# Kernel tuning notes

Hardware: AMD Instinct MI355X
Metric: run time of the kernel (lower is better)

The kernel has to match this reference:

```python
import jax, jax.numpy as jnp
import numpy as np

B, T, DM = 1, 8192, 1024
DS, DC, EXP = 16, 4, 2
DI = DM * EXP  # 2048


def setup_inputs() -> dict:
    key = jax.random.key(0)
    ks = jax.random.split(key, 6)
    sc = lambda k, shape, s: jax.random.normal(k, shape, jnp.float32) * s
    return {
        "x": jax.random.normal(ks[0], (B, T, DM), jnp.float32),
        "W_in": sc(ks[1], (DM, 2 * DI), 0.02),        # stored [in, out]
        "conv_w": sc(ks[2], (DI, 1, DC), 0.2),        # depthwise conv weight (OIH)
        "conv_b": jnp.zeros((DI,), jnp.float32),
        "W_x": sc(ks[3], (DI, 2 * DS + 1), 0.02),     # stored [in, out]
        "A_log": jnp.log(jnp.arange(1, DS + 1, dtype=jnp.float32)),
        "D": jnp.ones((DI,), jnp.float32),
        "W_out": sc(ks[4], (DI, DM), 0.02),           # stored [in, out]
    }


def reference(x, W_in, conv_w, conv_b, W_x, A_log, D, W_out):
    Bq, Tq, _ = x.shape
    # input projection and gate split
    xz = x @ W_in                              # [B,T,2*DI]
    xc, z = jnp.split(xz, 2, axis=-1)          # each [B,T,DI]
    # causal depthwise conv1d (pad left DC-1 == torch pad both + truncate [:T])
    xcT = jnp.transpose(xc, (0, 2, 1))         # [B,DI,T]
    conv = jax.lax.conv_general_dilated(
        xcT, conv_w, window_strides=(1,), padding=[(DC - 1, 0)],
        feature_group_count=DI)
    conv = conv + conv_b[None, :, None]
    xs = jax.nn.silu(jnp.transpose(conv, (0, 2, 1)))   # [B,T,DI]
    # selective SSM parameters (single shared delta per timestep)
    x_dbl = xs @ W_x                           # [B,T,2N+1]
    delta = jax.nn.softplus(x_dbl[..., :1])    # [B,T,1]
    Bp = x_dbl[..., 1:1 + DS]                  # [B,T,N]
    Cp = x_dbl[..., 1 + DS:]                   # [B,T,N]
    A = -jnp.exp(A_log)                        # [N]
    A_bar = jnp.exp(delta * A)                 # [B,T,N]
    B_bar = delta * Bp                         # [B,T,N]

    def step(h, inp):
        a_t, b_t, x_t, c_t = inp               # [B,N],[B,N],[B,DI],[B,N]
        h = a_t[:, None, :] * h + b_t[:, None, :] * x_t[:, :, None]  # [B,DI,N]
        y_t = jnp.einsum('bdn,bn->bd', h, c_t)
        return h, y_t

    h0 = jnp.zeros((Bq, DI, DS), xs.dtype)
    seq = (jnp.swapaxes(A_bar, 0, 1), jnp.swapaxes(B_bar, 0, 1),
           jnp.swapaxes(xs, 0, 1), jnp.swapaxes(Cp, 0, 1))
    _, ys = jax.lax.scan(step, h0, seq)        # ys: [T,B,DI]
    y = jnp.swapaxes(ys, 0, 1) + D * xs        # [B,T,DI]
    y = y * jax.nn.silu(z)
    return y @ W_out                           # [B,T,DM]
```

## Files before the change

### kernel.cpp

```cpp
#include <hip/hip_runtime.h>
#include <hip/hip_bf16.h>

#define T_SEQ 8192
#define DMODEL 1024
#define DINNER 2048
#define NSTATE 16
#define NCH 128
#define CL 64

typedef __attribute__((ext_vector_type(8))) short bf16x8;
typedef __attribute__((ext_vector_type(4))) float f32x4;

__device__ __forceinline__ float bf2f(ushort u) {
  union { unsigned u; float f; } c; c.u = ((unsigned)u) << 16; return c.f;
}
__device__ __forceinline__ ushort f2bf(float f) {
  union { float f; unsigned u; } c; c.f = f;
  unsigned r = c.u + 0x7FFFu + ((c.u >> 16) & 1u);
  return (ushort)(r >> 16);
}

#define GLD16(dst, src) __builtin_amdgcn_global_load_lds( \
    (const __attribute__((address_space(1))) void*)(src), \
    (__attribute__((address_space(3))) void*)(dst), 16, 0, 0)

template<int N> __device__ __forceinline__ void waitcnt_vm() {
  asm volatile("s_waitcnt vmcnt(%0)" :: "i"(N) : "memory");
}
#define LGKM0() do { asm volatile("s_waitcnt lgkmcnt(0)" ::: "memory"); \
                     __builtin_amdgcn_sched_barrier(0); } while (0)
#define BAR() do { __builtin_amdgcn_sched_barrier(0); __builtin_amdgcn_s_barrier(); \
                   __builtin_amdgcn_sched_barrier(0); } while (0)

__global__ __launch_bounds__(256) void cast_bf16(const float* __restrict__ in,
                                                 ushort* __restrict__ out, int n4) {
  int i = blockIdx.x * 256 + threadIdx.x;
  if (i < n4) {
    float4 v = ((const float4*)in)[i];
    ushort4 o;
    o.x = f2bf(v.x); o.y = f2bf(v.y); o.z = f2bf(v.z); o.w = f2bf(v.w);
    ((ushort4*)out)[i] = o;
  }
}

__global__ __launch_bounds__(256) void transpose_bf16(const float* __restrict__ in,
                                                      ushort* __restrict__ out, int R, int C) {
  __shared__ float tile[32][33];
  int bx = blockIdx.x * 32;
  int by = blockIdx.y * 32;
  int x = threadIdx.x, y = threadIdx.y;
#pragma unroll
  for (int j = 0; j < 32; j += 8)
    tile[y + j][x] = in[(size_t)(by + y + j) * C + bx + x];
  __syncthreads();
#pragma unroll
  for (int j = 0; j < 32; j += 8)
    out[(size_t)(bx + y + j) * R + by + x] = f2bf(tile[x][y + j]);
}

__global__ __launch_bounds__(256) void wx_transpose_pad(const float* __restrict__ Wx,
                                                        ushort* __restrict__ wxT) {
  int idx = blockIdx.x * 256 + threadIdx.x;
  int j = idx >> 11;
  int k = idx & 2047;
  wxT[idx] = (j < 33) ? f2bf(Wx[k * 33 + j]) : (ushort)0;
}

template<int OUTMODE, int MR>
__global__ __launch_bounds__(512, 2)
void gemm8p(const ushort* __restrict__ A, const ushort* __restrict__ B,
            void* __restrict__ out0, void* __restrict__ out1,
            int N, int K, int MX) {
  constexpr int BM = MR * 32;
  constexpr int H = MR / 2;
  constexpr int AHL = BM / 128;
  constexpr int VM = 2 * AHL + 2;
  extern __shared__ __align__(16) char smem[];
  char* const sBr = smem + 2 * BM * 128;

  const int tid = threadIdx.x, lane = tid & 63, wid = tid >> 6;
  const int wm = wid >> 2, wn = wid & 3;
  const int xcd = blockIdx.x & 7, jb = blockIdx.x >> 3;
  const int mtile = xcd * MX + (jb % MX), ntile = jb / MX;
  const int mbase = mtile * BM, nbase = ntile * 256;
  const int NT = K >> 6;

  const int sr = tid >> 3;
  const int scol = ((tid & 7) ^ (sr & 7)) << 3;
  const ushort* pA = A + (size_t)(mbase + sr) * K + scol;
  const ushort* pB = B + (size_t)(nbase + sr) * K + scol;

  auto stgA = [&](int buf, int h, int tt) {
#pragma unroll
    for (int r = 0; r < AHL; ++r)
      GLD16(smem + buf * (BM * 128) + (h * (BM / 2) + r * 64) * 128 + wid * 1024,
            pA + (size_t)(h * (BM / 2) + r * 64) * K + (size_t)tt * 64);
  };
  auto stgB = [&](int buf, int h, int tt) {
#pragma unroll
    for (int r = 0; r < 2; ++r)
      GLD16(sBr + buf * 32768 + (h * 128 + r * 64) * 128 + wid * 1024,
            pB + (size_t)(h * 128 + r * 64) * K + (size_t)tt * 64);
  };

  const int frow = lane & 15, hh = lane >> 4;
  const int sw[2] = { ((hh) ^ (frow & 7)) << 4, ((4 + hh) ^ (frow & 7)) << 4 };
  const int arow = (wm * (MR * 16) + frow) * 128;
  const int brow = (wn * 64 + frow) * 128;

  f32x4 acc[MR][4];
#pragma unroll
  for (int m = 0; m < MR; ++m)
#pragma unroll
    for (int n = 0; n < 4; ++n) acc[m][n] = (f32x4){0.f, 0.f, 0.f, 0.f};

  stgA(0, 0, 0); stgA(0, 1, 0); stgB(0, 0, 0); stgB(0, 1, 0);
  if (NT > 1) { stgA(1, 0, 1); stgA(1, 1, 1); stgB(1, 0, 1); }
  waitcnt_vm<VM>();
  BAR();

  for (int t = 0; t < NT; ++t) {
    const int b = t & 1;
    const char* bA = smem + b * (BM * 128);
    const char* bB = sBr + b * 32768;
    bf16x8 alo[H][2], ahi[H][2], b01[2][2], b23[2][2];

#pragma unroll
    for (int m = 0; m < H; ++m)
#pragma unroll
      for (int kk = 0; kk < 2; ++kk)
        alo[m][kk] = *(const bf16x8*)(bA + arow + m * 2048 + sw[kk]);
#pragma unroll
    for (int n = 0; n < 2; ++n)
#pragma unroll
      for (int kk = 0; kk < 2; ++kk)
        b01[n][kk] = *(const bf16x8*)(bB + brow + n * 2048 + sw[kk]);
    if (t + 1 < NT) stgB((t + 1) & 1, 1, t + 1);
    BAR(); LGKM0();
    __builtin_amdgcn_s_setprio(1);
#pragma unroll
    for (int m = 0; m < H; ++m)
#pragma unroll
      for (int n = 0; n < 2; ++n)
#pragma unroll
        for (int kk = 0; kk < 2; ++kk)
          acc[m][n] = __builtin_amdgcn_mfma_f32_16x16x32_bf16(alo[m][kk], b01[n][kk], acc[m][n], 0, 0, 0);
    __builtin_amdgcn_s_setprio(0);
    BAR();

#pragma unroll
    for (int m = 0; m < H; ++m)
#pragma unroll
      for (int kk = 0; kk < 2; ++kk)
        ahi[m][kk] = *(const bf16x8*)(bA + arow + (H + m) * 2048 + sw[kk]);
    BAR(); LGKM0();
    __builtin_amdgcn_s_setprio(1);
#pragma unroll
    for (int m = 0; m < H; ++m)
#pragma unroll
      for (int n = 0; n < 2; ++n)
#pragma unroll
        for (int kk = 0; kk < 2; ++kk)
          acc[H + m][n] = __builtin_amdgcn_mfma_f32_16x16x32_bf16(ahi[m][kk], b01[n][kk], acc[H + m][n], 0, 0, 0);
    __builtin_amdgcn_s_setprio(0);
    BAR();

#pragma unroll
    for (int n = 0; n < 2; ++n)
#pragma unroll
      for (int kk = 0; kk < 2; ++kk)
        b23[n][kk] = *(const bf16x8*)(bB + brow + (2 + n) * 2048 + sw[kk]);
    if (t + 2 < NT) stgA(b, 0, t + 2);
    BAR(); LGKM0();
    __builtin_amdgcn_s_setprio(1);
#pragma unroll
    for (int m = 0; m < H; ++m)
#pragma unroll
      for (int n = 0; n < 2; ++n)
#pragma unroll
        for (int kk = 0; kk < 2; ++kk)
          acc[H + m][2 + n] = __builtin_amdgcn_mfma_f32_16x16x32_bf16(ahi[m][kk], b23[n][kk], acc[H + m][2 + n], 0, 0, 0);
    __builtin_amdgcn_s_setprio(0);
    BAR();

    if (t + 2 < NT) { stgA(b, 1, t + 2); stgB(b, 0, t + 2); }
    __builtin_amdgcn_s_setprio(1);
#pragma unroll
    for (int m = 0; m < H; ++m)
#pragma unroll
      for (int n = 0; n < 2; ++n)
#pragma unroll
        for (int kk = 0; kk < 2; ++kk)
          acc[m][2 + n] = __builtin_amdgcn_mfma_f32_16x16x32_bf16(alo[m][kk], b23[n][kk], acc[m][2 + n], 0, 0, 0);
    __builtin_amdgcn_s_setprio(0);
    if (t + 2 < NT) waitcnt_vm<VM>(); else waitcnt_vm<0>();
    BAR();
  }

  const int crow0 = mbase + wm * (MR * 16) + (lane >> 4) * 4;
  const int ccol0 = wn * 64 + (lane & 15);
  if (OUTMODE == 0) {
    float* po = (float*)out0;
#pragma unroll
    for (int m = 0; m < MR; ++m)
#pragma unroll
      for (int n = 0; n < 4; ++n)
#pragma unroll
        for (int j = 0; j < 4; ++j)
          po[(size_t)(crow0 + m * 16 + j) * N + nbase + ccol0 + n * 16] = acc[m][n][j];
  } else {
    ushort* dst = (nbase < 2048) ? (ushort*)out0 : (ushort*)out1;
    const int cbase = (nbase & 2047) + ccol0;
#pragma unroll
    for (int m = 0; m < MR; ++m)
#pragma unroll
      for (int n = 0; n < 4; ++n)
#pragma unroll
        for (int j = 0; j < 4; ++j)
          dst[(size_t)(crow0 + m * 16 + j) * 2048 + cbase + n * 16] = f2bf(acc[m][n][j]);
  }
}

__global__ __launch_bounds__(256) void gemm_thin(const ushort* __restrict__ A,
                                                 const ushort* __restrict__ Bw,
                                                 float* __restrict__ part) {
  __shared__ __align__(16) ushort sA[128 * 64];
  __shared__ __align__(16) ushort sB[48 * 64];
  const int tid = threadIdx.x, lane = tid & 63, wid = tid >> 6;
  const int mbase = blockIdx.x * 128;
  const int kbase = blockIdx.y * 512;
  const int frow = lane & 15, fke = (lane >> 4) * 8;

  f32x4 acc[2][3];
#pragma unroll
  for (int m = 0; m < 2; ++m)
#pragma unroll
    for (int n = 0; n < 3; ++n) acc[m][n] = (f32x4){0.f, 0.f, 0.f, 0.f};

  for (int k0 = 0; k0 < 512; k0 += 64) {
#pragma unroll
    for (int j = 0; j < 4; ++j) {
      int o = tid * 16 + j * 4096;
      int row = o >> 7, ke = ((o >> 4) & 7) * 8;
      GLD16((char*)sA + wid * 1024 + j * 4096,
            A + (size_t)(mbase + row) * DINNER + kbase + k0 + ke);
    }
    for (int i = tid; i < 384; i += 256) {
      int brow = i >> 3, kc = (i & 7) * 8;
      *(bf16x8*)&sB[brow * 64 + kc] = *(const bf16x8*)(Bw + (size_t)brow * DINNER + kbase + k0 + kc);
    }
    __syncthreads();
    bf16x8 af[2][2], bf_[3][2];
#pragma unroll
    for (int m = 0; m < 2; ++m)
#pragma unroll
      for (int ks = 0; ks < 2; ++ks)
        af[m][ks] = *(const bf16x8*)&sA[(wid * 32 + m * 16 + frow) * 64 + ks * 32 + fke];
#pragma unroll
    for (int n = 0; n < 3; ++n)
#pragma unroll
      for (int ks = 0; ks < 2; ++ks)
        bf_[n][ks] = *(const bf16x8*)&sB[(n * 16 + frow) * 64 + ks * 32 + fke];
#pragma unroll
    for (int m = 0; m < 2; ++m)
#pragma unroll
      for (int n = 0; n < 3; ++n)
#pragma unroll
        for (int ks = 0; ks < 2; ++ks)
          acc[m][n] = __builtin_amdgcn_mfma_f32_16x16x32_bf16(af[m][ks], bf_[n][ks], acc[m][n], 0, 0, 0);
    __syncthreads();
  }
  float* po = part + (size_t)blockIdx.y * (T_SEQ * 48);
#pragma unroll
  for (int m = 0; m < 2; ++m)
#pragma unroll
    for (int n = 0; n < 3; ++n)
#pragma unroll
      for (int j = 0; j < 4; ++j) {
        int rr = mbase + wid * 32 + m * 16 + (lane >> 4) * 4 + j;
        int cc = n * 16 + (lane & 15);
        po[(size_t)rr * 48 + cc] = acc[m][n][j];
      }
}

__global__ __launch_bounds__(256) void reduce4(const float* __restrict__ part,
                                               float* __restrict__ xdbl) {
  int i = blockIdx.x * 256 + threadIdx.x;
  const float4* p = (const float4*)part;
  float4 a = p[i], b = p[i + 98304], c = p[i + 2 * 98304], d = p[i + 3 * 98304];
  ((float4*)xdbl)[i] = make_float4(a.x + b.x + c.x + d.x, a.y + b.y + c.y + d.y,
                                   a.z + b.z + c.z + d.z, a.w + b.w + c.w + d.w);
}

__global__ __launch_bounds__(256) void conv_silu(const ushort* __restrict__ xc,
                                                 const float* __restrict__ cw,
                                                 const float* __restrict__ cb,
                                                 ushort* __restrict__ xs) {
  int idx = blockIdx.x * 256 + threadIdx.x;
  int t = idx >> 11, d = idx & 2047;
  float4 w = *(const float4*)(cw + d * 4);
  float a = cb[d];
  const float wk[4] = {w.x, w.y, w.z, w.w};
#pragma unroll
  for (int k = 0; k < 4; ++k) {
    int tt = t - 3 + k;
    if (tt >= 0) a += bf2f(xc[(size_t)tt * 2048 + d]) * wk[k];
  }
  float s = a / (1.f + expf(-a));
  xs[idx] = f2bf(s);
}

__global__ __launch_bounds__(256) void precompute_k(const float* __restrict__ xdbl,
                                                    const float* __restrict__ A_log,
                                                    float* __restrict__ abar,
                                                    float* __restrict__ bbar,
                                                    float* __restrict__ cc,
                                                    float* __restrict__ dlt) {
  int t = blockIdx.x * 256 + threadIdx.x;
  if (t >= T_SEQ) return;
  const float* r = xdbl + (size_t)t * 48;
  float v = r[0];
  float delta = (v > 20.f) ? v : log1pf(expf(v));
  dlt[t] = delta;
#pragma unroll
  for (int n = 0; n < NSTATE; ++n) {
    float A = -expf(A_log[n]);
    abar[t * 16 + n] = expf(delta * A);
    bbar[t * 16 + n] = delta * r[1 + n];
    cc[t * 16 + n]   = r[17 + n];
  }
}

__global__ __launch_bounds__(256) void chunkprod_k(const float* __restrict__ dlt,
                                                   const float* __restrict__ A_log,
                                                   float* __restrict__ P) {
  int idx = blockIdx.x * 256 + threadIdx.x;
  if (idx >= NCH * NSTATE) return;
  int c = idx >> 4, n = idx & 15;
  float s = 0.f;
  for (int i = 0; i < CL; ++i) s += dlt[c * CL + i];
  P[idx] = expf(-expf(A_log[n]) * s);
}

__global__ __launch_bounds__(256) void scan1(const ushort* __restrict__ xs,
                                             const float* __restrict__ abar,
                                             const float* __restrict__ bbar,
                                             float* __restrict__ hend) {
  int c = blockIdx.x;
  int d = blockIdx.y * 256 + threadIdx.x;
  __shared__ float s_ab[CL * 16], s_bb[CL * 16];
  for (int e = threadIdx.x; e < CL * 16; e += 256) {
    s_ab[e] = abar[(size_t)c * CL * 16 + e];
    s_bb[e] = bbar[(size_t)c * CL * 16 + e];
  }
  __syncthreads();
  float h[16];
#pragma unroll
  for (int n = 0; n < 16; ++n) h[n] = 0.f;
  int tbase = c * CL;
  for (int i = 0; i < CL; ++i) {
    float x = bf2f(xs[(size_t)(tbase + i) * DINNER + d]);
#pragma unroll
    for (int n = 0; n < 16; ++n) h[n] = s_ab[i * 16 + n] * h[n] + s_bb[i * 16 + n] * x;
  }
  float* o = hend + ((size_t)c * DINNER + d) * 16;
#pragma unroll
  for (int qq = 0; qq < 4; ++qq)
    ((float4*)o)[qq] = make_float4(h[4 * qq], h[4 * qq + 1], h[4 * qq + 2], h[4 * qq + 3]);
}

__global__ __launch_bounds__(256) void scan2(const float* __restrict__ hend,
                                             const float* __restrict__ P,
                                             float* __restrict__ hin) {
  int idx = blockIdx.x * 256 + threadIdx.x;
  int n = idx & 15;
  float h = 0.f;
  for (int c = 0; c < NCH; ++c) {
    hin[(size_t)c * (DINNER * 16) + idx] = h;
    h = P[c * 16 + n] * h + hend[(size_t)c * (DINNER * 16) + idx];
  }
}

__global__ __launch_bounds__(256) void scan3(const ushort* __restrict__ xs,
                                             const ushort* __restrict__ zb,
                                             const float* __restrict__ abar,
                                             const float* __restrict__ bbar,
                                             const float* __restrict__ cc,
                                             const float* __restrict__ hin,
                                             const float* __restrict__ Dv,
                                             ushort* __restrict__ y) {
  int c = blockIdx.x;
  int d = blockIdx.y * 256 + threadIdx.x;
  __shared__ float s_ab[CL * 16], s_bb[CL * 16], s_cc[CL * 16];
  for (int e = threadIdx.x; e < CL * 16; e += 256) {
    s_ab[e] = abar[(size_t)c * CL * 16 + e];
    s_bb[e] = bbar[(size_t)c * CL * 16 + e];
    s_cc[e] = cc[(size_t)c * CL * 16 + e];
  }
  __syncthreads();
  float h[16];
  const float* hi = hin + ((size_t)c * DINNER + d) * 16;
#pragma unroll
  for (int qq = 0; qq < 4; ++qq) {
    float4 v = ((const float4*)hi)[qq];
    h[4 * qq] = v.x; h[4 * qq + 1] = v.y; h[4 * qq + 2] = v.z; h[4 * qq + 3] = v.w;
  }
  float Dd = Dv[d];
  int tbase = c * CL;
  for (int i = 0; i < CL; ++i) {
    size_t t = tbase + i;
    float x = bf2f(xs[t * DINNER + d]);
    float ys = 0.f;
#pragma unroll
    for (int n = 0; n < 16; ++n) {
      h[n] = s_ab[i * 16 + n] * h[n] + s_bb[i * 16 + n] * x;
      ys += s_cc[i * 16 + n] * h[n];
    }
    float z = bf2f(zb[t * 2048 + d]);
    float yv = (ys + Dd * x) * (z / (1.f + expf(-z)));
    y[t * DINNER + d] = f2bf(yv);
  }
}

extern "C" void kernel_launch(void* const* d_in, const int* in_sizes, int n_in,
                              void* d_out, int out_size, void* d_ws, size_t ws_size,
                              hipStream_t stream) {
  const float* x      = (const float*)d_in[0];
  const float* W_in   = (const float*)d_in[1];
  const float* conv_w = (const float*)d_in[2];
  const float* conv_b = (const float*)d_in[3];
  const float* W_x    = (const float*)d_in[4];
  const float* A_log  = (const float*)d_in[5];
  const float* Dv     = (const float*)d_in[6];
  const float* W_out  = (const float*)d_in[7];
  float* out = (float*)d_out;

  char* w = (char*)d_ws;
  auto alloc = [&](size_t bytes) { char* p = w; w += (bytes + 255) & ~(size_t)255; return p; };

  ushort* xbf   = (ushort*)alloc((size_t)T_SEQ * DMODEL * 2);
  ushort* winT  = (ushort*)alloc((size_t)4096 * 1024 * 2);
  ushort* woutT = (ushort*)alloc((size_t)1024 * 2048 * 2);
  ushort* wxT   = (ushort*)alloc((size_t)48 * 2048 * 2);
  ushort* xc    = (ushort*)alloc((size_t)T_SEQ * DINNER * 2);
  ushort* zb    = (ushort*)alloc((size_t)T_SEQ * DINNER * 2);
  ushort* xs    = (ushort*)alloc((size_t)T_SEQ * DINNER * 2);
  float*  xdbl  = (float*) alloc((size_t)T_SEQ * 48 * 4);
  float*  parts = (float*) alloc((size_t)4 * T_SEQ * 48 * 4);
  float*  abar  = (float*) alloc((size_t)T_SEQ * 16 * 4);
  float*  bbar  = (float*) alloc((size_t)T_SEQ * 16 * 4);
  float*  ccb   = (float*) alloc((size_t)T_SEQ * 16 * 4);
  float*  dlt   = (float*) alloc((size_t)T_SEQ * 4);
  float*  P     = (float*) alloc((size_t)NCH * 16 * 4);
  float*  hend  = (float*) alloc((size_t)NCH * DINNER * 16 * 4);
  float*  hin   = (float*) alloc((size_t)NCH * DINNER * 16 * 4);
  ushort* ybf   = (ushort*)alloc((size_t)T_SEQ * DINNER * 2);

  auto kg1 = gemm8p<1, 8>;
  auto kg3 = gemm8p<0, 4>;
  hipFuncSetAttribute(reinterpret_cast<const void*>(kg1),
                      hipFuncAttributeMaxDynamicSharedMemorySize, 131072);
  hipFuncSetAttribute(reinterpret_cast<const void*>(kg3),
                      hipFuncAttributeMaxDynamicSharedMemorySize, 98304);

  cast_bf16<<<(T_SEQ * DMODEL / 4 + 255) / 256, 256, 0, stream>>>(x, xbf, T_SEQ * DMODEL / 4);
  transpose_bf16<<<dim3(4096 / 32, 1024 / 32), dim3(32, 8), 0, stream>>>(W_in, winT, 1024, 4096);
  transpose_bf16<<<dim3(1024 / 32, 2048 / 32), dim3(32, 8), 0, stream>>>(W_out, woutT, 2048, 1024);
  wx_transpose_pad<<<(48 * 2048) / 256, 256, 0, stream>>>(W_x, wxT);

  kg1<<<dim3(512), 512, 131072, stream>>>(xbf, winT, xc, zb, 4096, 1024, 4);

  conv_silu<<<(T_SEQ * DINNER) / 256, 256, 0, stream>>>(xc, conv_w, conv_b, xs);

  gemm_thin<<<dim3(T_SEQ / 128, 4), 256, 0, stream>>>(xs, wxT, parts);
  reduce4<<<(T_SEQ * 48 / 4) / 256, 256, 0, stream>>>(parts, xdbl);

  precompute_k<<<T_SEQ / 256, 256, 0, stream>>>(xdbl, A_log, abar, bbar, ccb, dlt);
  chunkprod_k<<<(NCH * 16 + 255) / 256, 256, 0, stream>>>(dlt, A_log, P);

  scan1<<<dim3(NCH, DINNER / 256), 256, 0, stream>>>(xs, abar, bbar, hend);
  scan2<<<(DINNER * 16) / 256, 256, 0, stream>>>(hend, P, hin);
  scan3<<<dim3(NCH, DINNER / 256), 256, 0, stream>>>(xs, zb, abar, bbar, ccb, hin, Dv, ybf);

  kg3<<<dim3(256), 512, 98304, stream>>>(ybf, woutT, out, nullptr, 1024, 2048, 8);
}
```

Before: 298.6 us.

## Fuse prep kernels, fold reduce/chunkprod into precompute, store chunk states as bf16

Merges the cast and the three weight-transpose kernels into one launch, and folds the partial-sum reduction and the chunk decay-product computation into precompute_k using a shared-memory stage and wave shuffles. The inter-chunk states hend/hin are stored in bf16 instead of fp32. scan2 now batches its loads across 8 chunks at a time to give more memory-level parallelism. The aim is fewer launches and less memory traffic, in exchange for lower precision of the carried SSM state and a precompute launch of only 32 blocks.

```diff
diff --git a/kernel.cpp b/kernel.cpp
--- a/kernel.cpp
+++ b/kernel.cpp
@@ -29,41 +29,46 @@
 }
 #define LGKM0() do { asm volatile("s_waitcnt lgkmcnt(0)" ::: "memory"); \
                      __builtin_amdgcn_sched_barrier(0); } while (0)
-#define BAR() do { __builtin_amdgcn_sched_barrier(0); __builtin_amdgcn_s_barrier(); \
+#define BAR() do { __builtin_amdgcn_s_barrier(); \
                    __builtin_amdgcn_sched_barrier(0); } while (0)
 
-__global__ __launch_bounds__(256) void cast_bf16(const float* __restrict__ in,
-                                                 ushort* __restrict__ out, int n4) {
-  int i = blockIdx.x * 256 + threadIdx.x;
-  if (i < n4) {
-    float4 v = ((const float4*)in)[i];
+__global__ __launch_bounds__(256) void prep_all(const float* __restrict__ x,
+                                                const float* __restrict__ W_in,
+                                                const float* __restrict__ W_out,
+                                                const float* __restrict__ Wx,
+                                                ushort* __restrict__ xbf,
+                                                ushort* __restrict__ winT,
+                                                ushort* __restrict__ woutT,
+                                                ushort* __restrict__ wxT) {
+  __shared__ float tile[32][33];
+  int b = blockIdx.x, tid = threadIdx.x;
+  if (b < 8192) {
+    int i = b * 256 + tid;
+    float4 v = ((const float4*)x)[i];
     ushort4 o;
     o.x = f2bf(v.x); o.y = f2bf(v.y); o.z = f2bf(v.z); o.w = f2bf(v.w);
-    ((ushort4*)out)[i] = o;
-  }
-}
-
-__global__ __launch_bounds__(256) void transpose_bf16(const float* __restrict__ in,
-                                                      ushort* __restrict__ out, int R, int C) {
-  __shared__ float tile[32][33];
-  int bx = blockIdx.x * 32;
-  int by = blockIdx.y * 32;
-  int x = threadIdx.x, y = threadIdx.y;
+    ((ushort4*)xbf)[i] = o;
+    return;
+  }
+  b -= 8192;
+  const float* in; ushort* out; int R, C, bx, by;
+  if (b < 4096)      { in = W_in;  out = winT;  R = 1024; C = 4096; bx = b & 127; by = b >> 7; }
+  else if (b < 6144) { b -= 4096; in = W_out; out = woutT; R = 2048; C = 1024; bx = b & 31; by = b >> 5; }
+  else {
+    int idx = (b - 6144) * 256 + tid;
+    int j = idx >> 11, k = idx & 2047;
+    wxT[idx] = (j < 33) ? f2bf(Wx[k * 33 + j]) : (ushort)0;
+    return;
+  }
+  int xx = tid & 31, yy = tid >> 5;
+  bx *= 32; by *= 32;
 #pragma unroll
   for (int j = 0; j < 32; j += 8)
-    tile[y + j][x] = in[(size_t)(by + y + j) * C + bx + x];
+    tile[yy + j][xx] = in[(size_t)(by + yy + j) * C + bx + xx];
   __syncthreads();
 #pragma unroll
   for (int j = 0; j < 32; j += 8)
-    out[(size_t)(bx + y + j) * R + by + x] = f2bf(tile[x][y + j]);
-}
-
-__global__ __launch_bounds__(256) void wx_transpose_pad(const float* __restrict__ Wx,
-                                                        ushort* __restrict__ wxT) {
-  int idx = blockIdx.x * 256 + threadIdx.x;
-  int j = idx >> 11;
-  int k = idx & 2047;
-  wxT[idx] = (j < 33) ? f2bf(Wx[k * 33 + j]) : (ushort)0;
+    out[(size_t)(bx + yy + j) * R + by + xx] = f2bf(tile[xx][yy + j]);
 }
 
 template<int OUTMODE, int MR>
@@ -283,15 +288,6 @@
       }
 }
 
-__global__ __launch_bounds__(256) void reduce4(const float* __restrict__ part,
-                                               float* __restrict__ xdbl) {
-  int i = blockIdx.x * 256 + threadIdx.x;
-  const float4* p = (const float4*)part;
-  float4 a = p[i], b = p[i + 98304], c = p[i + 2 * 98304], d = p[i + 3 * 98304];
-  ((float4*)xdbl)[i] = make_float4(a.x + b.x + c.x + d.x, a.y + b.y + c.y + d.y,
-                                   a.z + b.z + c.z + d.z, a.w + b.w + c.w + d.w);
-}
-
 __global__ __launch_bounds__(256) void conv_silu(const ushort* __restrict__ xc,
                                                  const float* __restrict__ cw,
                                                  const float* __restrict__ cb,
@@ -310,18 +306,25 @@
   xs[idx] = f2bf(s);
 }
 
-__global__ __launch_bounds__(256) void precompute_k(const float* __restrict__ xdbl,
+__global__ __launch_bounds__(256) void precompute_k(const float* __restrict__ part,
                                                     const float* __restrict__ A_log,
                                                     float* __restrict__ abar,
                                                     float* __restrict__ bbar,
                                                     float* __restrict__ cc,
-                                                    float* __restrict__ dlt) {
-  int t = blockIdx.x * 256 + threadIdx.x;
-  if (t >= T_SEQ) return;
-  const float* r = xdbl + (size_t)t * 48;
+                                                    float* __restrict__ P) {
+  __shared__ float ld[256 * 33];
+  const int t0 = blockIdx.x * 256, tid = threadIdx.x;
+  for (int i = tid; i < 256 * 33; i += 256) {
+    int r = i / 33, col = i - r * 33;
+    size_t off = (size_t)(t0 + r) * 48 + col;
+    ld[i] = part[off] + part[(size_t)T_SEQ * 48 + off] +
+            part[2 * (size_t)T_SEQ * 48 + off] + part[3 * (size_t)T_SEQ * 48 + off];
+  }
+  __syncthreads();
+  const float* r = &ld[tid * 33];
   float v = r[0];
   float delta = (v > 20.f) ? v : log1pf(expf(v));
-  dlt[t] = delta;
+  int t = t0 + tid;
 #pragma unroll
   for (int n = 0; n < NSTATE; ++n) {
     float A = -expf(A_log[n]);
@@ -329,23 +332,18 @@
     bbar[t * 16 + n] = delta * r[1 + n];
     cc[t * 16 + n]   = r[17 + n];
   }
-}
-
-__global__ __launch_bounds__(256) void chunkprod_k(const float* __restrict__ dlt,
-                                                   const float* __restrict__ A_log,
-                                                   float* __restrict__ P) {
-  int idx = blockIdx.x * 256 + threadIdx.x;
-  if (idx >= NCH * NSTATE) return;
-  int c = idx >> 4, n = idx & 15;
-  float s = 0.f;
-  for (int i = 0; i < CL; ++i) s += dlt[c * CL + i];
-  P[idx] = expf(-expf(A_log[n]) * s);
+  float s = delta;
+#pragma unroll
+  for (int off = 32; off > 0; off >>= 1) s += __shfl_down(s, off);
+  s = __shfl(s, 0);
+  int lane = tid & 63, c = blockIdx.x * 4 + (tid >> 6);
+  if (lane < 16) P[c * 16 + lane] = expf(-expf(A_log[lane]) * s);
 }
 
 __global__ __launch_bounds__(256) void scan1(const ushort* __restrict__ xs,
                                              const float* __restrict__ abar,
                                              const float* __restrict__ bbar,
-                                             float* __restrict__ hend) {
+                                             ushort* __restrict__ hend) {
   int c = blockIdx.x;
   int d = blockIdx.y * 256 + threadIdx.x;
   __shared__ float s_ab[CL * 16], s_bb[CL * 16];
@@ -363,21 +361,32 @@
 #pragma unroll
     for (int n = 0; n < 16; ++n) h[n] = s_ab[i * 16 + n] * h[n] + s_bb[i * 16 + n] * x;
   }
-  float* o = hend + ((size_t)c * DINNER + d) * 16;
-#pragma unroll
-  for (int qq = 0; qq < 4; ++qq)
-    ((float4*)o)[qq] = make_float4(h[4 * qq], h[4 * qq + 1], h[4 * qq + 2], h[4 * qq + 3]);
-}
-
-__global__ __launch_bounds__(256) void scan2(const float* __restrict__ hend,
+  ushort* o = hend + ((size_t)c * DINNER + d) * 16;
+  bf16x8 o0, o1;
+#pragma unroll
+  for (int q = 0; q < 8; ++q) { o0[q] = (short)f2bf(h[q]); o1[q] = (short)f2bf(h[8 + q]); }
+  *(bf16x8*)o = o0;
+  *(bf16x8*)(o + 8) = o1;
+}
+
+__global__ __launch_bounds__(128) void scan2(const ushort* __restrict__ hend,
                                              const float* __restrict__ P,
-                                             float* __restrict__ hin) {
-  int idx = blockIdx.x * 256 + threadIdx.x;
+                                             ushort* __restrict__ hin) {
+  int idx = blockIdx.x * 128 + threadIdx.x;
   int n = idx & 15;
   float h = 0.f;
-  for (int c = 0; c < NCH; ++c) {
-    hin[(size_t)c * (DINNER * 16) + idx] = h;
-    h = P[c * 16 + n] * h + hend[(size_t)c * (DINNER * 16) + idx];
+  for (int g = 0; g < 16; ++g) {
+    float e[8], p[8];
+#pragma unroll
+    for (int j = 0; j < 8; ++j) {
+      e[j] = bf2f(hend[(size_t)(g * 8 + j) * 32768 + idx]);
+      p[j] = P[(g * 8 + j) * 16 + n];
+    }
+#pragma unroll
+    for (int j = 0; j < 8; ++j) {
+      hin[(size_t)(g * 8 + j) * 32768 + idx] = f2bf(h);
+      h = p[j] * h + e[j];
+    }
   }
 }
 
@@ -386,7 +395,7 @@
                                              const float* __restrict__ abar,
                                              const float* __restrict__ bbar,
                                              const float* __restrict__ cc,
-                                             const float* __restrict__ hin,
+                                             const ushort* __restrict__ hin,
                                              const float* __restrict__ Dv,
                                              ushort* __restrict__ y) {
   int c = blockIdx.x;
@@ -399,12 +408,10 @@
   }
   __syncthreads();
   float h[16];
-  const float* hi = hin + ((size_t)c * DINNER + d) * 16;
-#pragma unroll
-  for (int qq = 0; qq < 4; ++qq) {
-    float4 v = ((const float4*)hi)[qq];
-    h[4 * qq] = v.x; h[4 * qq + 1] = v.y; h[4 * qq + 2] = v.z; h[4 * qq + 3] = v.w;
-  }
+  const ushort* hi = hin + ((size_t)c * DINNER + d) * 16;
+  bf16x8 h0 = *(const bf16x8*)hi, h1 = *(const bf16x8*)(hi + 8);
+#pragma unroll
+  for (int q = 0; q < 8; ++q) { h[q] = bf2f((ushort)h0[q]); h[8 + q] = bf2f((ushort)h1[q]); }
   float Dd = Dv[d];
   int tbase = c * CL;
   for (int i = 0; i < CL; ++i) {
@@ -445,15 +452,13 @@
   ushort* xc    = (ushort*)alloc((size_t)T_SEQ * DINNER * 2);
   ushort* zb    = (ushort*)alloc((size_t)T_SEQ * DINNER * 2);
   ushort* xs    = (ushort*)alloc((size_t)T_SEQ * DINNER * 2);
-  float*  xdbl  = (float*) alloc((size_t)T_SEQ * 48 * 4);
   float*  parts = (float*) alloc((size_t)4 * T_SEQ * 48 * 4);
   float*  abar  = (float*) alloc((size_t)T_SEQ * 16 * 4);
   float*  bbar  = (float*) alloc((size_t)T_SEQ * 16 * 4);
   float*  ccb   = (float*) alloc((size_t)T_SEQ * 16 * 4);
-  float*  dlt   = (float*) alloc((size_t)T_SEQ * 4);
   float*  P     = (float*) alloc((size_t)NCH * 16 * 4);
-  float*  hend  = (float*) alloc((size_t)NCH * DINNER * 16 * 4);
-  float*  hin   = (float*) alloc((size_t)NCH * DINNER * 16 * 4);
+  ushort* hend  = (ushort*)alloc((size_t)NCH * DINNER * 16 * 2);
+  ushort* hin   = (ushort*)alloc((size_t)NCH * DINNER * 16 * 2);
   ushort* ybf   = (ushort*)alloc((size_t)T_SEQ * DINNER * 2);
 
   auto kg1 = gemm8p<1, 8>;
@@ -463,23 +468,18 @@
   hipFuncSetAttribute(reinterpret_cast<const void*>(kg3),
                       hipFuncAttributeMaxDynamicSharedMemorySize, 98304);
 
-  cast_bf16<<<(T_SEQ * DMODEL / 4 + 255) / 256, 256, 0, stream>>>(x, xbf, T_SEQ * DMODEL / 4);
-  transpose_bf16<<<dim3(4096 / 32, 1024 / 32), dim3(32, 8), 0, stream>>>(W_in, winT, 1024, 4096);
-  transpose_bf16<<<dim3(1024 / 32, 2048 / 32), dim3(32, 8), 0, stream>>>(W_out, woutT, 2048, 1024);
-  wx_transpose_pad<<<(48 * 2048) / 256, 256, 0, stream>>>(W_x, wxT);
+  prep_all<<<dim3(14720), 256, 0, stream>>>(x, W_in, W_out, W_x, xbf, winT, woutT, wxT);
 
   kg1<<<dim3(512), 512, 131072, stream>>>(xbf, winT, xc, zb, 4096, 1024, 4);
 
   conv_silu<<<(T_SEQ * DINNER) / 256, 256, 0, stream>>>(xc, conv_w, conv_b, xs);
 
   gemm_thin<<<dim3(T_SEQ / 128, 4), 256, 0, stream>>>(xs, wxT, parts);
-  reduce4<<<(T_SEQ * 48 / 4) / 256, 256, 0, stream>>>(parts, xdbl);
-
-  precompute_k<<<T_SEQ / 256, 256, 0, stream>>>(xdbl, A_log, abar, bbar, ccb, dlt);
-  chunkprod_k<<<(NCH * 16 + 255) / 256, 256, 0, stream>>>(dlt, A_log, P);
+
+  precompute_k<<<32, 256, 0, stream>>>(parts, A_log, abar, bbar, ccb, P);
 
   scan1<<<dim3(NCH, DINNER / 256), 256, 0, stream>>>(xs, abar, bbar, hend);
-  scan2<<<(DINNER * 16) / 256, 256, 0, stream>>>(hend, P, hin);
+  scan2<<<256, 128, 0, stream>>>(hend, P, hin);
   scan3<<<dim3(NCH, DINNER / 256), 256, 0, stream>>>(xs, zb, abar, bbar, ccb, hin, Dv, ybf);
 
   kg3<<<dim3(256), 512, 98304, stream>>>(ybf, woutT, out, nullptr, 1024, 2048, 8);
```

Result: faster. 285.2 us (-4.5%).
